# Performance work log

Hardware: AMD Instinct MI355X
Metric: run time of the kernel (lower is better)

Reference implementation:

```python
import jax, jax.numpy as jnp
import numpy as np

E, CAP, D, F = 8, 4096, 1024, 4096  # experts, capacity/expert, d_model, d_ff


def setup_inputs() -> dict:
    key = jax.random.key(0)
    k0, k1, k2 = jax.random.split(key, 3)
    inputs = jax.random.normal(k0, (1, E * CAP, D), dtype=jnp.float32)
    # per-expert FFN params (stacked over expert axis)
    W1 = jax.random.normal(k1, (E, D, F), dtype=jnp.float32) * (1.0 / np.sqrt(D))
    b1 = jnp.zeros((E, F), dtype=jnp.float32)
    W2 = jax.random.normal(k2, (E, F, D), dtype=jnp.float32) * (1.0 / np.sqrt(F))
    b2 = jnp.zeros((E, D), dtype=jnp.float32)
    return {"inputs": inputs, "W1": W1, "b1": b1, "W2": W2, "b2": b2}


def reference(inputs, W1, b1, W2, b2):
    # inputs: [B, E*C, D]. chunk(dim=1) over E experts == reshape to [B, E, C, D].
    B, T, D_ = inputs.shape
    x = inputs.reshape(B, E, T // E, D_)  # [B, E, C, D]
    # grouped GEMM form of the per-expert loop: each expert applies its own FFN
    h = jax.nn.gelu(jnp.einsum('becd,edf->becf', x, W1) + b1[None, :, None, :])
    y = jnp.einsum('becf,efd->becd', h, W2) + b2[None, :, None, :]
    # cat over dim=1 == reshape back
    return y.reshape(B, T, D_)
```

## Files before the change

kernel.cpp:

```cpp
#include <hip/hip_runtime.h>
#include <stdint.h>

#define E_ 8
#define C_ 4096
#define D_ 1024
#define F_ 4096

typedef __attribute__((ext_vector_type(8))) short bf16x8;
typedef __attribute__((ext_vector_type(4))) float f32x4;
typedef __attribute__((ext_vector_type(8))) unsigned short u16x8;
typedef __attribute__((ext_vector_type(4))) unsigned short u16x4;

__device__ __forceinline__ unsigned short f2bf(float x) {
  union { float f; uint32_t u; } v; v.f = x;
  uint32_t r = v.u + 0x7FFFu + ((v.u >> 16) & 1u);
  return (unsigned short)(r >> 16);
}

__device__ __forceinline__ float gelu_f(float x) {
  float x3 = x * x * x;
  float u = 0.7978845608028654f * __builtin_fmaf(0.044715f, x3, x);
  float t = __expf(2.0f * u);
  float th = 1.0f - 2.0f / (t + 1.0f);
  return 0.5f * x * (1.0f + th);
}

__global__ void convert_bf16_kernel(const float* __restrict__ in,
                                    unsigned short* __restrict__ out, size_t n) {
  size_t i = ((size_t)blockIdx.x * blockDim.x + threadIdx.x) * 8;
  size_t stride = (size_t)gridDim.x * blockDim.x * 8;
  for (; i < n; i += stride) {
    float4 a = *(const float4*)(in + i);
    float4 b = *(const float4*)(in + i + 4);
    u16x8 o;
    o[0] = f2bf(a.x); o[1] = f2bf(a.y); o[2] = f2bf(a.z); o[3] = f2bf(a.w);
    o[4] = f2bf(b.x); o[5] = f2bf(b.y); o[6] = f2bf(b.z); o[7] = f2bf(b.w);
    *(u16x8*)(out + i) = o;
  }
}

__global__ void transpose_bf16_kernel(const float* __restrict__ in,
                                      unsigned short* __restrict__ out,
                                      int K, int N) {
  const int ge = blockIdx.z;
  const float* src = in + (size_t)ge * K * N;
  unsigned short* dst = out + (size_t)ge * K * N;
  __shared__ float tile[32][33];
  int t = threadIdx.x;
  int tx = t & 31, ty = t >> 5;
  int k0 = blockIdx.x * 32, n0 = blockIdx.y * 32;
#pragma unroll
  for (int p = 0; p < 4; ++p)
    tile[ty + p * 8][tx] = src[(size_t)(k0 + ty + p * 8) * N + n0 + tx];
  __syncthreads();
#pragma unroll
  for (int p = 0; p < 4; ++p)
    dst[(size_t)(n0 + ty + p * 8) * K + k0 + tx] = f2bf(tile[tx][ty + p * 8]);
}

typedef const __attribute__((address_space(1))) uint32_t* gas1_ptr;
typedef __attribute__((address_space(3))) uint32_t* las3_ptr;

__device__ __forceinline__ void async16(const void* g, void* l) {
  __builtin_amdgcn_global_load_lds((gas1_ptr)(uintptr_t)g, (las3_ptr)(uintptr_t)l,
                                   16, 0, 0);
}


#define SYNC_PRE(VM, LG) do { \
    __builtin_amdgcn_sched_barrier(0); \
    __builtin_amdgcn_s_barrier(); \
    asm volatile("s_waitcnt vmcnt(" #VM ") lgkmcnt(" #LG ")" ::: "memory"); \
    __builtin_amdgcn_sched_barrier(0); \
    __builtin_amdgcn_s_setprio(1); \
  } while (0)

#define SYNC_POST() do { \
    __builtin_amdgcn_s_setprio(0); \
    __builtin_amdgcn_sched_barrier(0); \
    __builtin_amdgcn_s_barrier(); \
    __builtin_amdgcn_sched_barrier(0); \
  } while (0)

template <int MODE>
__global__ __launch_bounds__(512, 2) void gemm256_kernel(
    const unsigned short* __restrict__ A,
    const unsigned short* __restrict__ B,
    const float* __restrict__ bias,
    void* __restrict__ Cout,
    int K, int N, int numM, int numN,
    size_t aStride, size_t bStride, size_t cStride, int biasStride) {
  __shared__ char lds[131072];
  char* ldsp = (char*)lds;

  const int NT = K >> 6;
  const int NITER = NT >> 1;

  int lin = blockIdx.x;
  int nwg = gridDim.x;
  int qq = nwg >> 3, rr8 = nwg & 7;
  int xcd = lin & 7, idx = lin >> 3;
  int wg = (xcd < rr8 ? xcd * (qq + 1) : rr8 * (qq + 1) + (xcd - rr8) * qq) + idx;
  int per = numM * numN;
  int e = wg / per;
  int rem = wg - e * per;
  int tm = rem % numM, tn = rem / numM;

  A += (size_t)e * aStride;
  B += (size_t)e * bStride;
  bias += (size_t)e * biasStride;

  const int rowTile = tm << 8;
  const int colTile = tn << 8;

  const int tid = threadIdx.x;
  const int lane = tid & 63;
  const int w = tid >> 6;
  const int wm = w & 1, wn = w >> 1;
  const int l15 = lane & 15, q = lane >> 4;

  const size_t ldB = (size_t)K * 2;

  const int rlo = tid >> 3, kc = tid & 7;
  const int swzsrc = ((kc ^ (rlo & 7)) << 4);
  const int vA = (int)(rlo * (int)ldB) + swzsrc;
  const int bcol = (rlo & 31) + ((rlo >> 5) << 6);
  const int vB = (int)(bcol * (int)ldB) + swzsrc;
  const int dA = tid * 16;
  const int dB = 32768 + (rlo & 31) * 128 + (rlo >> 5) * 8192 + kc * 16;
  const char* Ag = (const char*)A + (size_t)rowTile * ldB;
  const char* Bg = (const char*)B + (size_t)colTile * ldB;
  const size_t r128 = (size_t)128 * ldB;

#define STAGE_A(bb, Ah, kt) do { \
    size_t u = (size_t)((Ah) * 64) * ldB + (size_t)(kt) * 128; \
    async16(Ag + u + vA, ldsp + (bb) * 65536 + (Ah) * 8192 + dA); \
    async16(Ag + u + r128 + vA, \
            ldsp + (bb) * 65536 + (Ah) * 8192 + 16384 + dA); \
  } while (0)

#define STAGE_B(bb, Bh, kt) do { \
    size_t u = (size_t)((Bh) * 32) * ldB + (size_t)(kt) * 128; \
    async16(Bg + u + vB, ldsp + (bb) * 65536 + (Bh) * 4096 + dB); \
    async16(Bg + u + r128 + vB, \
            ldsp + (bb) * 65536 + (Bh) * 4096 + 16384 + dB); \
  } while (0)

  const int k0 = (q * 16) ^ ((l15 & 7) << 4);
  const int iA00 = wm * 16384 + l15 * 128 + k0;
  const int iA01 = iA00 ^ 64;
  const int iA10 = iA00 + 65536;
  const int iA11 = iA01 + 65536;
  const int iB00 = 32768 + wn * 8192 + l15 * 128 + k0;
  const int iB01 = iB00 ^ 64;
  const int iB10 = iB00 + 65536;
  const int iB11 = iB01 + 65536;

  bf16x8 aE[4][2], aO[4][2], bZ[2][2], bY[2][2];
  f32x4 acc[8][4];
#pragma unroll
  for (int m = 0; m < 8; ++m)
#pragma unroll
    for (int n = 0; n < 4; ++n) acc[m][n] = {0.f, 0.f, 0.f, 0.f};

#define READ_A(dst, b0, b1, mh) do { \
    _Pragma("unroll") for (int m4 = 0; m4 < 4; ++m4) { \
      dst[m4][0] = *(const bf16x8*)(ldsp + (b0) + (mh) * 8192 + m4 * 2048); \
      dst[m4][1] = *(const bf16x8*)(ldsp + (b1) + (mh) * 8192 + m4 * 2048); \
    } \
  } while (0)

#define READ_B(dst, b0, b1, nh) do { \
    _Pragma("unroll") for (int n2 = 0; n2 < 2; ++n2) { \
      dst[n2][0] = *(const bf16x8*)(ldsp + (b0) + (nh) * 4096 + n2 * 2048); \
      dst[n2][1] = *(const bf16x8*)(ldsp + (b1) + (nh) * 4096 + n2 * 2048); \
    } \
  } while (0)

#define MFMA_Q(mh, nh, AF, BF) do { \
    _Pragma("unroll") for (int m4 = 0; m4 < 4; ++m4) \
    _Pragma("unroll") for (int n2 = 0; n2 < 2; ++n2) \
    _Pragma("unroll") for (int ks = 0; ks < 2; ++ks) \
      acc[(mh) * 4 + m4][(nh) * 2 + n2] = \
          __builtin_amdgcn_mfma_f32_16x16x32_bf16( \
              BF[n2][ks], AF[m4][ks], acc[(mh) * 4 + m4][(nh) * 2 + n2], 0, 0, 0); \
  } while (0)

  STAGE_A(0, 0, 0); STAGE_B(0, 0, 0); STAGE_B(0, 1, 0); STAGE_A(0, 1, 0);
  STAGE_A(1, 0, 1); STAGE_B(1, 0, 1); STAGE_B(1, 1, 1);
  asm volatile("s_waitcnt vmcnt(6)" ::: "memory");
  __builtin_amdgcn_sched_barrier(0);
  __builtin_amdgcn_s_barrier();
  __builtin_amdgcn_sched_barrier(0);
  READ_A(aE, iA00, iA01, 0);
  READ_B(bZ, iB00, iB01, 0);

  for (int j = 0; j < NITER; ++j) {
    int t1 = 2 * j + 1;
    int t2 = 2 * j + 2; if (t2 > NT - 1) t2 = NT - 1;
    int t3 = 2 * j + 3; if (t3 > NT - 1) t3 = NT - 1;

    READ_B(bY, iB00, iB01, 1);
    STAGE_A(1, 1, t1);
    SYNC_PRE(8, 4); MFMA_Q(0, 0, aE, bZ); SYNC_POST();
    READ_A(aO, iA00, iA01, 1);
    STAGE_A(0, 0, t2);
    SYNC_PRE(8, 8); MFMA_Q(0, 1, aE, bY); SYNC_POST();
    STAGE_B(0, 0, t2);
    SYNC_PRE(8, 0); MFMA_Q(1, 0, aO, bZ); SYNC_POST();
    READ_A(aE, iA10, iA11, 0);
    READ_B(bZ, iB10, iB11, 0);
    STAGE_B(0, 1, t2);
    SYNC_PRE(8, 12); MFMA_Q(1, 1, aO, bY); SYNC_POST();
    READ_B(bY, iB10, iB11, 1);
    STAGE_A(0, 1, t2);
    SYNC_PRE(8, 4); MFMA_Q(0, 0, aE, bZ); SYNC_POST();
    READ_A(aO, iA10, iA11, 1);
    STAGE_A(1, 0, t3);
    SYNC_PRE(8, 8); MFMA_Q(0, 1, aE, bY); SYNC_POST();
    STAGE_B(1, 0, t3);
    SYNC_PRE(8, 0); MFMA_Q(1, 0, aO, bZ); SYNC_POST();
    READ_A(aE, iA00, iA01, 0);
    READ_B(bZ, iB00, iB01, 0);
    STAGE_B(1, 1, t3);
    SYNC_PRE(8, 12); MFMA_Q(1, 1, aO, bY); SYNC_POST();
  }
  asm volatile("s_waitcnt vmcnt(0) lgkmcnt(0)" ::: "memory");
  __builtin_amdgcn_sched_barrier(0);

#pragma unroll
  for (int mf = 0; mf < 8; ++mf) {
    int row = rowTile + wm * 128 + mf * 16 + l15;
#pragma unroll
    for (int nf = 0; nf < 4; ++nf) {
      int col = colTile + wn * 64 + nf * 16 + q * 4;
      float4 bv = *(const float4*)(bias + col);
      f32x4 v = acc[mf][nf];
      if constexpr (MODE == 1) {
        u16x4 o;
        o[0] = f2bf(gelu_f(v[0] + bv.x));
        o[1] = f2bf(gelu_f(v[1] + bv.y));
        o[2] = f2bf(gelu_f(v[2] + bv.z));
        o[3] = f2bf(gelu_f(v[3] + bv.w));
        *(u16x4*)((unsigned short*)Cout + (size_t)e * cStride +
                  (size_t)row * N + col) = o;
      } else {
        float4 o;
        o.x = v[0] + bv.x; o.y = v[1] + bv.y;
        o.z = v[2] + bv.z; o.w = v[3] + bv.w;
        *(float4*)((float*)Cout + (size_t)e * cStride + (size_t)row * N + col) = o;
      }
    }
  }
}

extern "C" void kernel_launch(void* const* d_in, const int* in_sizes, int n_in,
                              void* d_out, int out_size, void* d_ws, size_t ws_size,
                              hipStream_t stream) {
  const float* X = (const float*)d_in[0];
  const float* W1 = (const float*)d_in[1];
  const float* b1 = (const float*)d_in[2];
  const float* W2 = (const float*)d_in[3];
  const float* b2 = (const float*)d_in[4];
  float* Y = (float*)d_out;

  const size_t szX = (size_t)C_ * D_ * 2;
  const size_t szW1 = (size_t)F_ * D_ * 2;
  const size_t szW2 = (size_t)D_ * F_ * 2;
  const size_t szH = (size_t)C_ * F_ * 2;
  const size_t fixed = szX + szW1 + szW2;

  int g = 0;
  {
    const int cands[4] = {8, 4, 2, 1};
    for (int i = 0; i < 4; ++i)
      if ((fixed + szH) * (size_t)cands[i] <= ws_size) { g = cands[i]; break; }
  }
  int RC = C_;
  if (g == 0) {
    g = 1;
    size_t avail = ws_size > fixed ? ws_size - fixed : 0;
    RC = (int)(avail / ((size_t)F_ * 2));
    RC = (RC / 256) * 256;
    if (RC < 256) RC = 256;
    if (RC > C_) RC = C_;
  }

  unsigned short* XB = (unsigned short*)d_ws;
  unsigned short* W1T = XB + (size_t)g * C_ * D_;
  unsigned short* W2T = W1T + (size_t)g * F_ * D_;
  unsigned short* H = W2T + (size_t)g * D_ * F_;

  const int numN1 = F_ / 256;
  const int numN2 = D_ / 256;

  for (int e0 = 0; e0 < E_; e0 += g) {
    {
      size_t n = (size_t)g * C_ * D_;
      size_t nb = (n / 8 + 255) / 256;
      if (nb > 2048) nb = 2048;
      convert_bf16_kernel<<<dim3((unsigned)nb), 256, 0, stream>>>(
          X + (size_t)e0 * C_ * D_, XB, n);
    }
    transpose_bf16_kernel<<<dim3(D_ / 32, F_ / 32, g), 256, 0, stream>>>(
        W1 + (size_t)e0 * D_ * F_, W1T, D_, F_);
    transpose_bf16_kernel<<<dim3(F_ / 32, D_ / 32, g), 256, 0, stream>>>(
        W2 + (size_t)e0 * F_ * D_, W2T, F_, D_);

    for (int r0 = 0; r0 < C_; r0 += RC) {
      int numM = RC / 256;
      gemm256_kernel<1><<<dim3((unsigned)(numM * numN1 * g)), 512, 0, stream>>>(
          XB + (size_t)r0 * D_, W1T, b1 + (size_t)e0 * F_, (void*)H,
          D_, F_, numM, numN1,
          (size_t)C_ * D_, (size_t)F_ * D_, (size_t)RC * F_, F_);
      gemm256_kernel<0><<<dim3((unsigned)(numM * numN2 * g)), 512, 0, stream>>>(
          H, W2T, b2 + (size_t)e0 * D_,
          (void*)(Y + (size_t)e0 * C_ * D_ + (size_t)r0 * D_),
          F_, D_, numM, numN2,
          (size_t)RC * F_, (size_t)D_ * F_, (size_t)C_ * D_, D_);
    }
  }
}
```

Before: 849.4 us.

## Restructure GEMM main loop to single-tile-ahead prefetch with interleaved staging

Cuts the prologue from staging two K-tiles to staging one. The main loop now issues global-to-LDS staging for the next tile inside the same barrier-bracketed phases as the MFMA quarters and LDS fragment reads. The wait placement changes so vmcnt is awaited before the barrier and lgkmcnt(0) after it, which simplifies the dependency counting. This reduces prefetch depth, which may expose global load latency, in exchange for possibly less instruction-issue contention between phases.

Measured after the change: 751.9 us. -11.5%, faster.

```diff
diff --git a/kernel.cpp b/kernel.cpp
--- a/kernel.cpp
+++ b/kernel.cpp
@@ -67,15 +67,16 @@
 }
 
 
-#define SYNC_PRE(VM, LG) do { \
+#define PRE(VM) do { \
     __builtin_amdgcn_sched_barrier(0); \
+    asm volatile("s_waitcnt vmcnt(" #VM ")" ::: "memory"); \
     __builtin_amdgcn_s_barrier(); \
-    asm volatile("s_waitcnt vmcnt(" #VM ") lgkmcnt(" #LG ")" ::: "memory"); \
+    asm volatile("s_waitcnt lgkmcnt(0)" ::: "memory"); \
     __builtin_amdgcn_sched_barrier(0); \
     __builtin_amdgcn_s_setprio(1); \
   } while (0)
 
-#define SYNC_POST() do { \
+#define POST() do { \
     __builtin_amdgcn_s_setprio(0); \
     __builtin_amdgcn_sched_barrier(0); \
     __builtin_amdgcn_s_barrier(); \
@@ -187,8 +188,7 @@
   } while (0)
 
   STAGE_A(0, 0, 0); STAGE_B(0, 0, 0); STAGE_B(0, 1, 0); STAGE_A(0, 1, 0);
-  STAGE_A(1, 0, 1); STAGE_B(1, 0, 1); STAGE_B(1, 1, 1);
-  asm volatile("s_waitcnt vmcnt(6)" ::: "memory");
+  asm volatile("s_waitcnt vmcnt(0)" ::: "memory");
   __builtin_amdgcn_sched_barrier(0);
   __builtin_amdgcn_s_barrier();
   __builtin_amdgcn_sched_barrier(0);
@@ -198,32 +198,45 @@
   for (int j = 0; j < NITER; ++j) {
     int t1 = 2 * j + 1;
     int t2 = 2 * j + 2; if (t2 > NT - 1) t2 = NT - 1;
-    int t3 = 2 * j + 3; if (t3 > NT - 1) t3 = NT - 1;
-
+
+    PRE(2);
+    STAGE_A(1, 0, t1); STAGE_B(1, 0, t1);
     READ_B(bY, iB00, iB01, 1);
+    MFMA_Q(0, 0, aE, bZ);
+    POST();
+    PRE(4);
+    READ_A(aO, iA00, iA01, 1);
+    MFMA_Q(0, 1, aE, bY);
+    POST();
+    PRE(4);
+    STAGE_B(1, 1, t1);
+    MFMA_Q(1, 0, aO, bZ);
+    POST();
+    PRE(2);
     STAGE_A(1, 1, t1);
-    SYNC_PRE(8, 4); MFMA_Q(0, 0, aE, bZ); SYNC_POST();
-    READ_A(aO, iA00, iA01, 1);
-    STAGE_A(0, 0, t2);
-    SYNC_PRE(8, 8); MFMA_Q(0, 1, aE, bY); SYNC_POST();
-    STAGE_B(0, 0, t2);
-    SYNC_PRE(8, 0); MFMA_Q(1, 0, aO, bZ); SYNC_POST();
     READ_A(aE, iA10, iA11, 0);
     READ_B(bZ, iB10, iB11, 0);
+    MFMA_Q(1, 1, aO, bY);
+    POST();
+    PRE(2);
+    STAGE_A(0, 0, t2); STAGE_B(0, 0, t2);
+    READ_B(bY, iB10, iB11, 1);
+    MFMA_Q(0, 0, aE, bZ);
+    POST();
+    PRE(4);
+    READ_A(aO, iA10, iA11, 1);
+    MFMA_Q(0, 1, aE, bY);
+    POST();
+    PRE(4);
     STAGE_B(0, 1, t2);
-    SYNC_PRE(8, 12); MFMA_Q(1, 1, aO, bY); SYNC_POST();
-    READ_B(bY, iB10, iB11, 1);
+    MFMA_Q(1, 0, aO, bZ);
+    POST();
+    PRE(2);
     STAGE_A(0, 1, t2);
-    SYNC_PRE(8, 4); MFMA_Q(0, 0, aE, bZ); SYNC_POST();
-    READ_A(aO, iA10, iA11, 1);
-    STAGE_A(1, 0, t3);
-    SYNC_PRE(8, 8); MFMA_Q(0, 1, aE, bY); SYNC_POST();
-    STAGE_B(1, 0, t3);
-    SYNC_PRE(8, 0); MFMA_Q(1, 0, aO, bZ); SYNC_POST();
     READ_A(aE, iA00, iA01, 0);
     READ_B(bZ, iB00, iB01, 0);
-    STAGE_B(1, 1, t3);
-    SYNC_PRE(8, 12); MFMA_Q(1, 1, aO, bY); SYNC_POST();
+    MFMA_Q(1, 1, aO, bY);
+    POST();
   }
   asm volatile("s_waitcnt vmcnt(0) lgkmcnt(0)" ::: "memory");
   __builtin_amdgcn_sched_barrier(0);
```

## Interleave global staging and LDS reads between MFMAs inside each phase

Applied to the files above, without the earlier changes.

Restructures the main GEMM loop so each MFMA quadrant phase interleaves individual MFMA pairs with global-to-LDS staging and LDS fragment reads, fenced with sched_barriers. The prefetch depth drops from two K-tiles ahead to one, and the barrier waits become vmcnt before the barrier plus lgkmcnt(0) after it. The goal is to hide memory issue latency under matrix ops instead of issuing loads in bulk between phases. The shallower prefetch may expose more global-load latency.

Measured after the change: 815.4 us. 1.04x faster.

```diff
diff --git a/kernel.cpp b/kernel.cpp
--- a/kernel.cpp
+++ b/kernel.cpp
@@ -67,15 +67,18 @@
 }
 
 
-#define SYNC_PRE(VM, LG) do { \
+#define FEN() __builtin_amdgcn_sched_barrier(0)
+
+#define PRE(VM) do { \
     __builtin_amdgcn_sched_barrier(0); \
+    asm volatile("s_waitcnt vmcnt(" #VM ")" ::: "memory"); \
     __builtin_amdgcn_s_barrier(); \
-    asm volatile("s_waitcnt vmcnt(" #VM ") lgkmcnt(" #LG ")" ::: "memory"); \
+    asm volatile("s_waitcnt lgkmcnt(0)" ::: "memory"); \
     __builtin_amdgcn_sched_barrier(0); \
     __builtin_amdgcn_s_setprio(1); \
   } while (0)
 
-#define SYNC_POST() do { \
+#define POST() do { \
     __builtin_amdgcn_s_setprio(0); \
     __builtin_amdgcn_sched_barrier(0); \
     __builtin_amdgcn_s_barrier(); \
@@ -163,67 +166,87 @@
 #pragma unroll
     for (int n = 0; n < 4; ++n) acc[m][n] = {0.f, 0.f, 0.f, 0.f};
 
-#define READ_A(dst, b0, b1, mh) do { \
-    _Pragma("unroll") for (int m4 = 0; m4 < 4; ++m4) { \
-      dst[m4][0] = *(const bf16x8*)(ldsp + (b0) + (mh) * 8192 + m4 * 2048); \
-      dst[m4][1] = *(const bf16x8*)(ldsp + (b1) + (mh) * 8192 + m4 * 2048); \
-    } \
-  } while (0)
-
-#define READ_B(dst, b0, b1, nh) do { \
-    _Pragma("unroll") for (int n2 = 0; n2 < 2; ++n2) { \
-      dst[n2][0] = *(const bf16x8*)(ldsp + (b0) + (nh) * 4096 + n2 * 2048); \
-      dst[n2][1] = *(const bf16x8*)(ldsp + (b1) + (nh) * 4096 + n2 * 2048); \
-    } \
-  } while (0)
-
-#define MFMA_Q(mh, nh, AF, BF) do { \
-    _Pragma("unroll") for (int m4 = 0; m4 < 4; ++m4) \
-    _Pragma("unroll") for (int n2 = 0; n2 < 2; ++n2) \
-    _Pragma("unroll") for (int ks = 0; ks < 2; ++ks) \
-      acc[(mh) * 4 + m4][(nh) * 2 + n2] = \
-          __builtin_amdgcn_mfma_f32_16x16x32_bf16( \
-              BF[n2][ks], AF[m4][ks], acc[(mh) * 4 + m4][(nh) * 2 + n2], 0, 0, 0); \
+#define PR(mh, nh, AF, BF, m4, n2) do { \
+    acc[(mh)*4+(m4)][(nh)*2+(n2)] = __builtin_amdgcn_mfma_f32_16x16x32_bf16( \
+        BF[n2][0], AF[m4][0], acc[(mh)*4+(m4)][(nh)*2+(n2)], 0, 0, 0); \
+    acc[(mh)*4+(m4)][(nh)*2+(n2)] = __builtin_amdgcn_mfma_f32_16x16x32_bf16( \
+        BF[n2][1], AF[m4][1], acc[(mh)*4+(m4)][(nh)*2+(n2)], 0, 0, 0); \
+  } while (0)
+
+#define RA(dst, b0, b1, mh, m4) do { \
+    dst[m4][0] = *(const bf16x8*)(ldsp + (b0) + (mh) * 8192 + (m4) * 2048); \
+    dst[m4][1] = *(const bf16x8*)(ldsp + (b1) + (mh) * 8192 + (m4) * 2048); \
+  } while (0)
+
+#define RB(dst, b0, b1, nh, n2) do { \
+    dst[n2][0] = *(const bf16x8*)(ldsp + (b0) + (nh) * 4096 + (n2) * 2048); \
+    dst[n2][1] = *(const bf16x8*)(ldsp + (b1) + (nh) * 4096 + (n2) * 2048); \
+  } while (0)
+
+#define PH_Q00(AF, BF, BYd, cB0, cB1, sb, st) do { \
+    PRE(2); \
+    PR(0,0,AF,BF,0,0); FEN(); STAGE_A(sb,0,st); FEN(); \
+    PR(0,0,AF,BF,0,1); FEN(); STAGE_B(sb,0,st); FEN(); \
+    PR(0,0,AF,BF,1,0); FEN(); RB(BYd,cB0,cB1,1,0); FEN(); \
+    PR(0,0,AF,BF,1,1); FEN(); RB(BYd,cB0,cB1,1,1); FEN(); \
+    PR(0,0,AF,BF,2,0); PR(0,0,AF,BF,2,1); \
+    PR(0,0,AF,BF,3,0); PR(0,0,AF,BF,3,1); \
+    POST(); \
+  } while (0)
+
+#define PH_Q01(AF, BF, AOd, cA0, cA1) do { \
+    PRE(4); \
+    PR(0,1,AF,BF,0,0); FEN(); RA(AOd,cA0,cA1,1,0); FEN(); \
+    PR(0,1,AF,BF,0,1); FEN(); RA(AOd,cA0,cA1,1,1); FEN(); \
+    PR(0,1,AF,BF,1,0); FEN(); RA(AOd,cA0,cA1,1,2); FEN(); \
+    PR(0,1,AF,BF,1,1); FEN(); RA(AOd,cA0,cA1,1,3); FEN(); \
+    PR(0,1,AF,BF,2,0); PR(0,1,AF,BF,2,1); \
+    PR(0,1,AF,BF,3,0); PR(0,1,AF,BF,3,1); \
+    POST(); \
+  } while (0)
+
+#define PH_Q10(AF, BF, sb, st) do { \
+    PRE(4); \
+    PR(1,0,AF,BF,0,0); FEN(); STAGE_B(sb,1,st); FEN(); \
+    PR(1,0,AF,BF,0,1); PR(1,0,AF,BF,1,0); PR(1,0,AF,BF,1,1); \
+    PR(1,0,AF,BF,2,0); PR(1,0,AF,BF,2,1); \
+    PR(1,0,AF,BF,3,0); PR(1,0,AF,BF,3,1); \
+    POST(); \
+  } while (0)
+
+#define PH_Q11(AF, BF, AEd, BZd, nA0, nA1, nB0, nB1, sb, st) do { \
+    PRE(2); \
+    PR(1,1,AF,BF,0,0); FEN(); STAGE_A(sb,1,st); FEN(); \
+    PR(1,1,AF,BF,0,1); FEN(); RA(AEd,nA0,nA1,0,0); FEN(); \
+    PR(1,1,AF,BF,1,0); FEN(); RA(AEd,nA0,nA1,0,1); FEN(); \
+    PR(1,1,AF,BF,1,1); FEN(); RA(AEd,nA0,nA1,0,2); FEN(); \
+    PR(1,1,AF,BF,2,0); FEN(); RA(AEd,nA0,nA1,0,3); FEN(); \
+    PR(1,1,AF,BF,2,1); FEN(); RB(BZd,nB0,nB1,0,0); FEN(); \
+    PR(1,1,AF,BF,3,0); FEN(); RB(BZd,nB0,nB1,0,1); FEN(); \
+    PR(1,1,AF,BF,3,1); \
+    POST(); \
   } while (0)
 
   STAGE_A(0, 0, 0); STAGE_B(0, 0, 0); STAGE_B(0, 1, 0); STAGE_A(0, 1, 0);
-  STAGE_A(1, 0, 1); STAGE_B(1, 0, 1); STAGE_B(1, 1, 1);
-  asm volatile("s_waitcnt vmcnt(6)" ::: "memory");
+  asm volatile("s_waitcnt vmcnt(0)" ::: "memory");
   __builtin_amdgcn_sched_barrier(0);
   __builtin_amdgcn_s_barrier();
   __builtin_amdgcn_sched_barrier(0);
-  READ_A(aE, iA00, iA01, 0);
-  READ_B(bZ, iB00, iB01, 0);
+  RA(aE, iA00, iA01, 0, 0); RA(aE, iA00, iA01, 0, 1);
+  RA(aE, iA00, iA01, 0, 2); RA(aE, iA00, iA01, 0, 3);
+  RB(bZ, iB00, iB01, 0, 0); RB(bZ, iB00, iB01, 0, 1);
 
   for (int j = 0; j < NITER; ++j) {
     int t1 = 2 * j + 1;
     int t2 = 2 * j + 2; if (t2 > NT - 1) t2 = NT - 1;
-    int t3 = 2 * j + 3; if (t3 > NT - 1) t3 = NT - 1;
-
-    READ_B(bY, iB00, iB01, 1);
-    STAGE_A(1, 1, t1);
-    SYNC_PRE(8, 4); MFMA_Q(0, 0, aE, bZ); SYNC_POST();
-    READ_A(aO, iA00, iA01, 1);
-    STAGE_A(0, 0, t2);
-    SYNC_PRE(8, 8); MFMA_Q(0, 1, aE, bY); SYNC_POST();
-    STAGE_B(0, 0, t2);
-    SYNC_PRE(8, 0); MFMA_Q(1, 0, aO, bZ); SYNC_POST();
-    READ_A(aE, iA10, iA11, 0);
-    READ_B(bZ, iB10, iB11, 0);
-    STAGE_B(0, 1, t2);
-    SYNC_PRE(8, 12); MFMA_Q(1, 1, aO, bY); SYNC_POST();
-    READ_B(bY, iB10, iB11, 1);
-    STAGE_A(0, 1, t2);
-    SYNC_PRE(8, 4); MFMA_Q(0, 0, aE, bZ); SYNC_POST();
-    READ_A(aO, iA10, iA11, 1);
-    STAGE_A(1, 0, t3);
-    SYNC_PRE(8, 8); MFMA_Q(0, 1, aE, bY); SYNC_POST();
-    STAGE_B(1, 0, t3);
-    SYNC_PRE(8, 0); MFMA_Q(1, 0, aO, bZ); SYNC_POST();
-    READ_A(aE, iA00, iA01, 0);
-    READ_B(bZ, iB00, iB01, 0);
-    STAGE_B(1, 1, t3);
-    SYNC_PRE(8, 12); MFMA_Q(1, 1, aO, bY); SYNC_POST();
+    PH_Q00(aE, bZ, bY, iB00, iB01, 1, t1);
+    PH_Q01(aE, bY, aO, iA00, iA01);
+    PH_Q10(aO, bZ, 1, t1);
+    PH_Q11(aO, bY, aE, bZ, iA10, iA11, iB10, iB11, 1, t1);
+    PH_Q00(aE, bZ, bY, iB10, iB11, 0, t2);
+    PH_Q01(aE, bY, aO, iA10, iA11);
+    PH_Q10(aO, bZ, 0, t2);
+    PH_Q11(aO, bY, aE, bZ, iA00, iA01, iB00, iB01, 0, t2);
   }
   asm volatile("s_waitcnt vmcnt(0) lgkmcnt(0)" ::: "memory");
   __builtin_amdgcn_sched_barrier(0);
```
